# Optimization experiments

Hardware: AMD Instinct MI355X
Metric: run time of the kernel (lower is better)

## Reference

```python
import jax, jax.numpy as jnp
import numpy as np

B, H, W, C, NBHD, T, OUT_DIM = 4, 96, 96, 256, 48, 3025, 512
N = H * W
INNER = 4
DS_RATE = 0.25


def _layer_norm(x, w, b, eps=1e-5):
    mu = jnp.mean(x, axis=-1, keepdims=True)
    var = jnp.mean((x - mu) ** 2, axis=-1, keepdims=True)
    return (x - mu) * jax.lax.rsqrt(var + eps) * w + b


def setup_inputs() -> dict:
    key = jax.random.key(0)
    ks = jax.random.split(key, 8)
    # regular grid positions: pos % 4 == 0 (both dims) on exactly 24*24=576 tokens
    yy, xx = jnp.meshgrid(jnp.arange(H), jnp.arange(W), indexing='ij')
    pos = jnp.stack([yy, xx], axis=-1).reshape(1, N, 2).astype(jnp.float32)
    pos = jnp.broadcast_to(pos, (B, N, 2))
    feat = jax.random.normal(ks[0], (B, N, C), dtype=jnp.float32)
    member_idx = jax.random.randint(ks[1], (B, N, NBHD), 0, N)
    cluster_mask = (jax.random.uniform(ks[2], (B, N, NBHD)) > 0.1).astype(jnp.float32)
    learned_prob = jax.random.uniform(ks[3], (B, N, 1), dtype=jnp.float32)
    pe_idx = jax.random.randint(ks[4], (B, N, NBHD), 0, T)
    pre_table = jax.random.normal(ks[5], (T, 5), dtype=jnp.float32)
    # weight_net: Linear(5,4) + LayerNorm(4) + GELU
    w1 = jax.random.normal(ks[6], (5, INNER), dtype=jnp.float32) * 0.3
    b1 = jnp.zeros((INNER,), jnp.float32)
    ln1_w = jnp.ones((INNER,), jnp.float32)
    ln1_b = jnp.zeros((INNER,), jnp.float32)
    # norm over inner_ch*dim, then Linear(inner_ch*dim -> out_dim)
    norm_w = jnp.ones((INNER * C,), jnp.float32)
    norm_b = jnp.zeros((INNER * C,), jnp.float32)
    lin_w = jax.random.normal(ks[7], (INNER * C, OUT_DIM), dtype=jnp.float32) * 0.02
    lin_b = jnp.zeros((OUT_DIM,), jnp.float32)
    return {
        'pos': pos, 'feat': feat, 'member_idx': member_idx,
        'cluster_mask': cluster_mask, 'learned_prob': learned_prob,
        'pe_idx': pe_idx, 'pre_table': pre_table,
        'w1': w1, 'b1': b1, 'ln1_w': ln1_w, 'ln1_b': ln1_b,
        'norm_w': norm_w, 'norm_b': norm_b, 'lin_w': lin_w, 'lin_b': lin_b,
        'stride': 2, 'reserve_num': 576,
    }


def reference(pos, feat, member_idx, cluster_mask, learned_prob, pe_idx,
              pre_table, w1, b1, ln1_w, ln1_b, norm_w, norm_b, lin_w, lin_b,
              stride, reserve_num):
    b, n, c = feat.shape
    nbhd = member_idx.shape[-1]
    keep_num = int(n * DS_RATE)
    sample_num = keep_num - reserve_num

    pos_long = pos.astype(jnp.int32)
    lp_det = jax.lax.stop_gradient(learned_prob[..., 0])  # b x n (detached in torch)
    reserve_mask = jnp.all(pos_long % (stride * 2) == 0, axis=-1).astype(jnp.float32)
    final_prob = lp_det + reserve_mask * (-100.0)

    # topk sampled tokens (reserved tokens pushed to -100 so never sampled)
    sample_idx = jax.lax.top_k(final_prob, sample_num)[1]  # b x sample_num
    # reserved token indices in ascending index order (torch nonzero order)
    reserve_idx = jnp.argsort(-reserve_mask, axis=1, stable=True)[:, :reserve_num]
    idx = jnp.concatenate([sample_idx, reserve_idx], axis=1)  # b x keep_num

    pos_down = jnp.take_along_axis(pos, idx[:, :, None], axis=1)  # b x keep x 2

    member_d = jnp.take_along_axis(member_idx, idx[:, :, None], axis=1)   # b x keep x nbhd
    pe_d = jnp.take_along_axis(pe_idx, idx[:, :, None], axis=1)
    cmask_d = jnp.take_along_axis(cluster_mask, idx[:, :, None], axis=1)

    flat_mi = member_d.reshape(b, keep_num * nbhd)
    # gather learned prob of each neighbor (NOT detached: grads flow)
    lp_nb = jnp.take_along_axis(learned_prob, flat_mi[:, :, None], axis=1)
    lp_nb = lp_nb.reshape(b, keep_num, nbhd, 1)

    # weight_net over pre-computed position table -> T x inner_ch
    wt = jax.nn.gelu(_layer_norm(pre_table @ w1 + b1, ln1_w, ln1_b))
    weights = wt[pe_d]  # b x keep x nbhd x inner_ch
    weights = weights * (lp_nb * cmask_d[..., None])

    # gather neighbor features and do position-weighted aggregation
    feat_g = jnp.take_along_axis(feat, flat_mi[:, :, None], axis=1)
    feat_g = feat_g.reshape(b, keep_num, nbhd, c)
    feat_down = jnp.einsum('bnkm,bnkc->bnmc', weights, feat_g)
    feat_down = feat_down.reshape(b, keep_num, INNER * c)

    feat_down = _layer_norm(feat_down, norm_w, norm_b)
    feat_down = feat_down @ lin_w + lin_b
    return pos_down, feat_down
```

## Files before the change

kernel.cpp:

```cpp
#include <hip/hip_runtime.h>
#include <hip/hip_bf16.h>
#include <stdint.h>

#define BB 4
#define NN 9216
#define CC 256
#define NBHD 48
#define T_TAB 3025
#define OUT_DIM 512
#define KEEP 2304
#define RESERVE 576
#define SAMPLE 1728
#define W_IMG 96

typedef __attribute__((ext_vector_type(4))) float f32x4;
typedef __attribute__((ext_vector_type(8))) short s16x8;

__device__ inline unsigned short f2bf_bits(float x) {
    __hip_bfloat16 h = __float2bfloat16(x);
    return __builtin_bit_cast(unsigned short, h);
}

__global__ void wt_kernel(const float* __restrict__ pre_table,
                          const float* __restrict__ w1,
                          const float* __restrict__ b1,
                          const float* __restrict__ ln1w,
                          const float* __restrict__ ln1b,
                          float* __restrict__ wt) {
    int t = blockIdx.x * blockDim.x + threadIdx.x;
    if (t >= T_TAB) return;
    float p[5];
#pragma unroll
    for (int j = 0; j < 5; j++) p[j] = pre_table[t * 5 + j];
    float h[4];
#pragma unroll
    for (int m = 0; m < 4; m++) {
        float a = b1[m];
#pragma unroll
        for (int j = 0; j < 5; j++) a += p[j] * w1[j * 4 + m];
        h[m] = a;
    }
    float mu = 0.25f * (h[0] + h[1] + h[2] + h[3]);
    float var = 0.f;
#pragma unroll
    for (int m = 0; m < 4; m++) { float d = h[m] - mu; var += d * d; }
    var *= 0.25f;
    float rs = rsqrtf(var + 1e-5f);
#pragma unroll
    for (int m = 0; m < 4; m++) {
        float x = (h[m] - mu) * rs * ln1w[m] + ln1b[m];
        float u = 0.7978845608028654f * (x + 0.044715f * x * x * x);
        wt[t * 4 + m] = 0.5f * x * (1.0f + tanhf(u));
    }
}

#define JSPLIT 8
#define JCHUNK (NN / JSPLIT)
__device__ inline float final_prob(const float* f, int i) {
    int y = i / W_IMG, x = i % W_IMG;
    bool res = ((y & 3) == 0) && ((x & 3) == 0);
    return f[i] + (res ? -100.0f : 0.0f);
}
__global__ __launch_bounds__(256) void rank_kernel(const float* __restrict__ lp,
                                                   int* __restrict__ rank) {
    __shared__ float s[JCHUNK];
    int b = blockIdx.z;
    int i = blockIdx.x * 256 + threadIdx.x;
    int jbase = blockIdx.y * JCHUNK;
    const float* f = lp + b * NN;
    for (int j = threadIdx.x; j < JCHUNK; j += 256)
        s[j] = final_prob(f, jbase + j);
    __syncthreads();
    float fi = final_prob(f, i);
    int cnt = 0;
#pragma unroll 8
    for (int jj = 0; jj < JCHUNK; jj++) {
        float fj = s[jj];
        int j = jbase + jj;
        cnt += (int)((fj > fi) || (fj == fi && j < i));
    }
    atomicAdd(&rank[b * NN + i], cnt);
}

__global__ void scatter_kernel(const float* __restrict__ pos,
                               const int* __restrict__ rank,
                               int* __restrict__ idx,
                               float* __restrict__ pos_down) {
    int g = blockIdx.x * 256 + threadIdx.x;
    if (g >= BB * NN) return;
    int b = g / NN, i = g % NN;
    float py = pos[g * 2 + 0], px = pos[g * 2 + 1];
    int y = (int)py, x = (int)px;
    bool res = ((y & 3) == 0) && ((x & 3) == 0);
    int slot = -1;
    if (res) {
        slot = SAMPLE + (y >> 2) * (W_IMG / 4) + (x >> 2);
    } else {
        int r = rank[g];
        if (r < SAMPLE) slot = r;
    }
    if (slot >= 0) {
        idx[b * KEEP + slot] = i;
        pos_down[(b * KEEP + slot) * 2 + 0] = py;
        pos_down[(b * KEEP + slot) * 2 + 1] = px;
    }
}

__global__ void feat2bf_kernel(const float* __restrict__ f,
                               unsigned short* __restrict__ o) {
    int g = blockIdx.x * 256 + threadIdx.x;
    float4 v = ((const float4*)f)[g];
    ushort4 u;
    u.x = f2bf_bits(v.x); u.y = f2bf_bits(v.y);
    u.z = f2bf_bits(v.z); u.w = f2bf_bits(v.w);
    ((ushort4*)o)[g] = u;
}

__global__ __launch_bounds__(256) void wtrans_kernel(const float* __restrict__ W,
                                                     __hip_bfloat16* __restrict__ Wt) {
    __shared__ float s[32][33];
    int bx = blockIdx.x;
    int by = blockIdx.y;
    int tx = threadIdx.x & 31, ty = threadIdx.x >> 5;
#pragma unroll
    for (int r = 0; r < 4; r++)
        s[ty * 4 + r][tx] = W[(size_t)(by * 32 + ty * 4 + r) * 512 + bx * 32 + tx];
    __syncthreads();
#pragma unroll
    for (int r = 0; r < 4; r++)
        Wt[(size_t)(bx * 32 + ty * 4 + r) * 1024 + by * 32 + tx] =
            __float2bfloat16(s[tx][ty * 4 + r]);
}

__device__ inline float ldf(const float* p) { return *p; }
__device__ inline float ldf(const __hip_bfloat16* p) { return __bfloat162float(*p); }

template <typename FT>
__global__ __launch_bounds__(256) void agg_kernel(
        const FT* __restrict__ feat,
        const int* __restrict__ member_idx,
        const float* __restrict__ cmask,
        const float* __restrict__ lp,
        const int* __restrict__ pe_idx,
        const float* __restrict__ wt,
        const int* __restrict__ idx,
        const float* __restrict__ norm_w,
        const float* __restrict__ norm_b,
        __hip_bfloat16* __restrict__ xnorm) {
    int t = blockIdx.x, b = blockIdx.y, tid = threadIdx.x;
    __shared__ int s_mem[NBHD];
    __shared__ float s_w[NBHD * 4];
    __shared__ float s_red[8];
    int i = idx[b * KEEP + t];
    if (tid < NBHD) {
        size_t base = ((size_t)b * NN + i) * NBHD + tid;
        int mi = member_idx[base];
        int pe = pe_idx[base];
        float fsc = lp[b * NN + mi] * cmask[base];
        s_mem[tid] = mi;
        s_w[tid * 4 + 0] = wt[pe * 4 + 0] * fsc;
        s_w[tid * 4 + 1] = wt[pe * 4 + 1] * fsc;
        s_w[tid * 4 + 2] = wt[pe * 4 + 2] * fsc;
        s_w[tid * 4 + 3] = wt[pe * 4 + 3] * fsc;
    }
    __syncthreads();
    float a0 = 0.f, a1 = 0.f, a2 = 0.f, a3 = 0.f;
    const FT* fb = feat + (size_t)b * NN * CC + tid;
#pragma unroll 4
    for (int k = 0; k < NBHD; k++) {
        float fv = ldf(fb + (size_t)s_mem[k] * CC);
        a0 += s_w[k * 4 + 0] * fv;
        a1 += s_w[k * 4 + 1] * fv;
        a2 += s_w[k * 4 + 2] * fv;
        a3 += s_w[k * 4 + 3] * fv;
    }
    float s1 = a0 + a1 + a2 + a3;
    float s2 = a0 * a0 + a1 * a1 + a2 * a2 + a3 * a3;
    for (int off = 32; off > 0; off >>= 1) {
        s1 += __shfl_down(s1, off);
        s2 += __shfl_down(s2, off);
    }
    int wid = tid >> 6;
    if ((tid & 63) == 0) { s_red[wid] = s1; s_red[4 + wid] = s2; }
    __syncthreads();
    float S1 = s_red[0] + s_red[1] + s_red[2] + s_red[3];
    float S2 = s_red[4] + s_red[5] + s_red[6] + s_red[7];
    float mu = S1 * (1.0f / 1024.0f);
    float var = S2 * (1.0f / 1024.0f) - mu * mu;
    float rs = rsqrtf(var + 1e-5f);
    __hip_bfloat16* xo = xnorm + ((size_t)(b * KEEP + t)) * 1024;
#pragma unroll
    for (int m = 0; m < 4; m++) {
        float am = (m == 0) ? a0 : (m == 1) ? a1 : (m == 2) ? a2 : a3;
        int c = m * 256 + tid;
        xo[c] = __float2bfloat16((am - mu) * rs * norm_w[c] + norm_b[c]);
    }
}

__device__ inline void async16(const void* g, void* l) {
    __builtin_amdgcn_global_load_lds(
        (const __attribute__((address_space(1))) void*)g,
        (__attribute__((address_space(3))) void*)l, 16, 0, 0);
}
__device__ inline void mfma16x16x32(f32x4& d, const s16x8& a, const s16x8& b) {
    asm("v_mfma_f32_16x16x32_bf16 %0, %1, %2, %0" : "+v"(d) : "v"(a), "v"(b));
}

__global__ __launch_bounds__(256) void mfma_gemm(
        const __hip_bfloat16* __restrict__ A,
        const __hip_bfloat16* __restrict__ Bt,
        const float* __restrict__ bias,
        float* __restrict__ Cout) {
    __shared__ __hip_bfloat16 sA[128 * 32];
    __shared__ __hip_bfloat16 sB[128 * 32];
    int tid = threadIdx.x;
    int wave = tid >> 6, lane = tid & 63;
    int wm = wave >> 1, wn = wave & 1;
    int row0 = blockIdx.y * 128, col0 = blockIdx.x * 128;

    int lrow = lane >> 2;
    int lcol = (lane & 3) * 8;
    const __hip_bfloat16* gA = A + (size_t)(row0 + wave * 32 + lrow) * 1024 + lcol;
    const __hip_bfloat16* gB = Bt + (size_t)(col0 + wave * 32 + lrow) * 1024 + lcol;
    __hip_bfloat16* lA0 = sA + (wave * 32) * 32;
    __hip_bfloat16* lA1 = sA + (wave * 32 + 16) * 32;
    __hip_bfloat16* lB0 = sB + (wave * 32) * 32;
    __hip_bfloat16* lB1 = sB + (wave * 32 + 16) * 32;

    f32x4 acc[4][4] = {};
    int fr = lane & 15;
    int fq = lane >> 4;

    for (int kk = 0; kk < 1024; kk += 32) {
        async16(gA + kk, lA0);
        async16(gA + kk + 16 * 1024, lA1);
        async16(gB + kk, lB0);
        async16(gB + kk + 16 * 1024, lB1);
        __syncthreads();
        s16x8 af[4], bf[4];
#pragma unroll
        for (int i = 0; i < 4; i++)
            af[i] = *(const s16x8*)(sA + (wm * 64 + i * 16 + fr) * 32 + fq * 8);
#pragma unroll
        for (int j = 0; j < 4; j++)
            bf[j] = *(const s16x8*)(sB + (wn * 64 + j * 16 + fr) * 32 + fq * 8);
#pragma unroll
        for (int i = 0; i < 4; i++)
#pragma unroll
            for (int j = 0; j < 4; j++)
                mfma16x16x32(acc[i][j], af[i], bf[j]);
        __syncthreads();
    }
    asm volatile("s_nop 7\ns_nop 7" ::);
    float bv[4];
#pragma unroll
    for (int j = 0; j < 4; j++) bv[j] = bias[col0 + wn * 64 + j * 16 + fr];
#pragma unroll
    for (int i = 0; i < 4; i++) {
        int row = row0 + wm * 64 + i * 16 + fq * 4;
#pragma unroll
        for (int j = 0; j < 4; j++) {
            int col = col0 + wn * 64 + j * 16 + fr;
            float* cp = Cout + (size_t)row * 512 + col;
#pragma unroll
            for (int r = 0; r < 4; r++)
                cp[(size_t)r * 512] = acc[i][j][r] + bv[j];
        }
    }
}

extern "C" void kernel_launch(void* const* d_in, const int* in_sizes, int n_in,
                              void* d_out, int out_size, void* d_ws, size_t ws_size,
                              hipStream_t stream) {
    const float* pos       = (const float*)d_in[0];
    const float* feat      = (const float*)d_in[1];
    const int*   member_idx= (const int*)d_in[2];
    const float* cmask     = (const float*)d_in[3];
    const float* lp        = (const float*)d_in[4];
    const int*   pe_idx    = (const int*)d_in[5];
    const float* pre_table = (const float*)d_in[6];
    const float* w1        = (const float*)d_in[7];
    const float* b1        = (const float*)d_in[8];
    const float* ln1w      = (const float*)d_in[9];
    const float* ln1b      = (const float*)d_in[10];
    const float* norm_w    = (const float*)d_in[11];
    const float* norm_b    = (const float*)d_in[12];
    const float* lin_w     = (const float*)d_in[13];
    const float* lin_b     = (const float*)d_in[14];

    float* out = (float*)d_out;
    float* pos_down = out;
    float* feat_out = out + (size_t)BB * KEEP * 2;

    char* ws = (char*)d_ws;
    float*          wt     = (float*)(ws + 0);
    int*            rank   = (int*)  (ws + 48640);
    int*            idx    = (int*)  (ws + 196096);
    __hip_bfloat16* wtb    = (__hip_bfloat16*)(ws + 232960);
    __hip_bfloat16* xnormb = (__hip_bfloat16*)(ws + 1281536);
    __hip_bfloat16* featb  = (__hip_bfloat16*)(ws + 20155904);
    const size_t NEED_BF16FEAT = 20155904 + 18874368;
    bool use_bf16_feat = (ws_size >= NEED_BF16FEAT);

    wt_kernel<<<dim3((T_TAB + 255) / 256), 256, 0, stream>>>(pre_table, w1, b1, ln1w, ln1b, wt);
    hipMemsetAsync(rank, 0, (size_t)BB * NN * 4, stream);
    rank_kernel<<<dim3(NN / 256, JSPLIT, BB), 256, 0, stream>>>(lp, rank);
    scatter_kernel<<<dim3((BB * NN) / 256), 256, 0, stream>>>(pos, rank, idx, pos_down);
    wtrans_kernel<<<dim3(512 / 32, 1024 / 32), 256, 0, stream>>>(lin_w, wtb);
    if (use_bf16_feat) {
        feat2bf_kernel<<<dim3((BB * NN * CC / 4) / 256), 256, 0, stream>>>(feat, (unsigned short*)featb);
        agg_kernel<__hip_bfloat16><<<dim3(KEEP, BB), 256, 0, stream>>>(
            featb, member_idx, cmask, lp, pe_idx, wt, idx, norm_w, norm_b, xnormb);
    } else {
        agg_kernel<float><<<dim3(KEEP, BB), 256, 0, stream>>>(
            feat, member_idx, cmask, lp, pe_idx, wt, idx, norm_w, norm_b, xnormb);
    }
    mfma_gemm<<<dim3(OUT_DIM / 128, (BB * KEEP) / 128), 256, 0, stream>>>(xnormb, wtb, lin_b, feat_out);
}
```

Before: 254.1 us.

## Replace all-pairs rank with histogram threshold and candidate ranking for top-k

Replaces the O(N^2) all-pairs rank counting over every token with a radix-histogram top-k selection. A 16-bit key histogram sets a threshold bin, candidates at or above it are gathered with atomics, and only those candidates are ranked pairwise. Positions are now derived from the token index instead of read from pos. This relies on the candidate count staying under CAND_CAP, which learned_prob values clustered in one bin could exceed, and it adds several small serial launches.

Result: slower. 355.8 us (+40.0%).

```diff
diff --git a/kernel.cpp b/kernel.cpp
--- a/kernel.cpp
+++ b/kernel.cpp
@@ -12,6 +12,7 @@
 #define RESERVE 576
 #define SAMPLE 1728
 #define W_IMG 96
+#define CAND_CAP 6144
 
 typedef __attribute__((ext_vector_type(4))) float f32x4;
 typedef __attribute__((ext_vector_type(8))) short s16x8;
@@ -19,6 +20,16 @@
 __device__ inline unsigned short f2bf_bits(float x) {
     __hip_bfloat16 h = __float2bfloat16(x);
     return __builtin_bit_cast(unsigned short, h);
+}
+
+__device__ inline unsigned int fkey(float v) {
+    unsigned int u = __builtin_bit_cast(unsigned int, v);
+    return (u & 0x80000000u) ? ~u : (u | 0x80000000u);
+}
+__device__ inline float final_prob_val(const float* lpb, int i) {
+    int y = i / W_IMG, x = i % W_IMG;
+    bool res = ((y & 3) == 0) && ((x & 3) == 0);
+    return lpb[i] + (res ? -100.0f : 0.0f);
 }
 
 __global__ void wt_kernel(const float* __restrict__ pre_table,
@@ -54,55 +65,108 @@
     }
 }
 
-#define JSPLIT 8
-#define JCHUNK (NN / JSPLIT)
-__device__ inline float final_prob(const float* f, int i) {
-    int y = i / W_IMG, x = i % W_IMG;
-    bool res = ((y & 3) == 0) && ((x & 3) == 0);
-    return f[i] + (res ? -100.0f : 0.0f);
-}
-__global__ __launch_bounds__(256) void rank_kernel(const float* __restrict__ lp,
-                                                   int* __restrict__ rank) {
-    __shared__ float s[JCHUNK];
-    int b = blockIdx.z;
-    int i = blockIdx.x * 256 + threadIdx.x;
-    int jbase = blockIdx.y * JCHUNK;
-    const float* f = lp + b * NN;
-    for (int j = threadIdx.x; j < JCHUNK; j += 256)
-        s[j] = final_prob(f, jbase + j);
+__global__ void hist_kernel(const float* __restrict__ lp,
+                            int* __restrict__ hist) {
+    int g = blockIdx.x * 256 + threadIdx.x;
+    if (g >= BB * NN) return;
+    int b = g / NN, i = g % NN;
+    float v = final_prob_val(lp + b * NN, i);
+    unsigned int bin = fkey(v) >> 16;
+    atomicAdd(&hist[b * 65536 + bin], 1);
+}
+
+__global__ __launch_bounds__(256) void thresh_kernel(const int* __restrict__ hist,
+                                                     int* __restrict__ thr) {
+    int b = blockIdx.x, t = threadIdx.x;
+    __shared__ int part[256];
+    const int* h = hist + b * 65536;
+    int lo = 65536 - (t + 1) * 256;
+    int sum = 0;
+    for (int k = 0; k < 256; k++) sum += h[lo + k];
+    part[t] = sum;
     __syncthreads();
-    float fi = final_prob(f, i);
-    int cnt = 0;
-#pragma unroll 8
-    for (int jj = 0; jj < JCHUNK; jj++) {
-        float fj = s[jj];
-        int j = jbase + jj;
-        cnt += (int)((fj > fi) || (fj == fi && j < i));
-    }
-    atomicAdd(&rank[b * NN + i], cnt);
-}
-
-__global__ void scatter_kernel(const float* __restrict__ pos,
-                               const int* __restrict__ rank,
+    if (t == 0) {
+        int cum = 0, T = 0;
+        for (int r = 0; r < 256; r++) {
+            if (cum + part[r] >= SAMPLE) {
+                int lo2 = 65536 - (r + 1) * 256;
+                int c = cum;
+                for (int bin = 65536 - r * 256 - 1; bin >= lo2; bin--) {
+                    c += h[bin];
+                    if (c >= SAMPLE) { T = bin; break; }
+                }
+                break;
+            }
+            cum += part[r];
+        }
+        thr[b] = T;
+    }
+}
+
+__global__ void collect_kernel(const float* __restrict__ lp,
+                               const int* __restrict__ thr,
+                               int* __restrict__ cnt,
+                               float* __restrict__ cand_val,
+                               int* __restrict__ cand_idx,
                                int* __restrict__ idx,
                                float* __restrict__ pos_down) {
     int g = blockIdx.x * 256 + threadIdx.x;
     if (g >= BB * NN) return;
     int b = g / NN, i = g % NN;
-    float py = pos[g * 2 + 0], px = pos[g * 2 + 1];
-    int y = (int)py, x = (int)px;
+    int y = i / W_IMG, x = i % W_IMG;
     bool res = ((y & 3) == 0) && ((x & 3) == 0);
-    int slot = -1;
     if (res) {
-        slot = SAMPLE + (y >> 2) * (W_IMG / 4) + (x >> 2);
+        int slot = SAMPLE + (y >> 2) * (W_IMG / 4) + (x >> 2);
+        idx[b * KEEP + slot] = i;
+        pos_down[(b * KEEP + slot) * 2 + 0] = (float)y;
+        pos_down[(b * KEEP + slot) * 2 + 1] = (float)x;
     } else {
-        int r = rank[g];
-        if (r < SAMPLE) slot = r;
-    }
-    if (slot >= 0) {
-        idx[b * KEEP + slot] = i;
-        pos_down[(b * KEEP + slot) * 2 + 0] = py;
-        pos_down[(b * KEEP + slot) * 2 + 1] = px;
+        float v = lp[g];
+        if ((int)(fkey(v) >> 16) >= thr[b]) {
+            int p = atomicAdd(&cnt[b], 1);
+            if (p < CAND_CAP) {
+                cand_val[b * CAND_CAP + p] = v;
+                cand_idx[b * CAND_CAP + p] = i;
+            }
+        }
+    }
+}
+
+#define RCHUNK 2048
+__global__ __launch_bounds__(256) void rank_cand_kernel(
+        const int* __restrict__ cnt,
+        const float* __restrict__ cand_val,
+        const int* __restrict__ cand_idx,
+        int* __restrict__ idx,
+        float* __restrict__ pos_down) {
+    __shared__ float sv[RCHUNK];
+    __shared__ int si[RCHUNK];
+    int b = blockIdx.y;
+    int C = cnt[b]; if (C > CAND_CAP) C = CAND_CAP;
+    int i = blockIdx.x * 256 + threadIdx.x;
+    bool valid = (i < C);
+    float vi = 0.f; int ii = 0;
+    if (valid) { vi = cand_val[b * CAND_CAP + i]; ii = cand_idx[b * CAND_CAP + i]; }
+    int rank = 0;
+    for (int base = 0; base < C; base += RCHUNK) {
+        int len = min(RCHUNK, C - base);
+        for (int j = threadIdx.x; j < len; j += 256) {
+            sv[j] = cand_val[b * CAND_CAP + base + j];
+            si[j] = cand_idx[b * CAND_CAP + base + j];
+        }
+        __syncthreads();
+        if (valid) {
+            for (int j = 0; j < len; j++) {
+                float vj = sv[j];
+                rank += (int)((vj > vi) || (vj == vi && si[j] < ii));
+            }
+        }
+        __syncthreads();
+    }
+    if (valid && rank < SAMPLE) {
+        idx[b * KEEP + rank] = ii;
+        pos_down[(b * KEEP + rank) * 2 + 0] = (float)(ii / W_IMG);
+        pos_down[(b * KEEP + rank) * 2 + 1] = (float)(ii % W_IMG);
     }
 }
 
@@ -294,18 +358,24 @@
 
     char* ws = (char*)d_ws;
     float*          wt     = (float*)(ws + 0);
-    int*            rank   = (int*)  (ws + 48640);
-    int*            idx    = (int*)  (ws + 196096);
-    __hip_bfloat16* wtb    = (__hip_bfloat16*)(ws + 232960);
-    __hip_bfloat16* xnormb = (__hip_bfloat16*)(ws + 1281536);
-    __hip_bfloat16* featb  = (__hip_bfloat16*)(ws + 20155904);
-    const size_t NEED_BF16FEAT = 20155904 + 18874368;
+    int*            hist   = (int*)  (ws + 48640);
+    int*            ccnt   = (int*)  (ws + 1097216);
+    int*            thr    = (int*)  (ws + 1097472);
+    float*          cval   = (float*)(ws + 1097728);
+    int*            cidx   = (int*)  (ws + 1196032);
+    int*            idx    = (int*)  (ws + 1294336);
+    __hip_bfloat16* wtb    = (__hip_bfloat16*)(ws + 1331200);
+    __hip_bfloat16* xnormb = (__hip_bfloat16*)(ws + 2379776);
+    __hip_bfloat16* featb  = (__hip_bfloat16*)(ws + 21254144);
+    const size_t NEED_BF16FEAT = 21254144 + 18874368;
     bool use_bf16_feat = (ws_size >= NEED_BF16FEAT);
 
     wt_kernel<<<dim3((T_TAB + 255) / 256), 256, 0, stream>>>(pre_table, w1, b1, ln1w, ln1b, wt);
-    hipMemsetAsync(rank, 0, (size_t)BB * NN * 4, stream);
-    rank_kernel<<<dim3(NN / 256, JSPLIT, BB), 256, 0, stream>>>(lp, rank);
-    scatter_kernel<<<dim3((BB * NN) / 256), 256, 0, stream>>>(pos, rank, idx, pos_down);
+    hipMemsetAsync(hist, 0, 1048576 + 256, stream);
+    hist_kernel<<<dim3((BB * NN) / 256), 256, 0, stream>>>(lp, hist);
+    thresh_kernel<<<dim3(BB), 256, 0, stream>>>(hist, thr);
+    collect_kernel<<<dim3((BB * NN) / 256), 256, 0, stream>>>(lp, thr, ccnt, cval, cidx, idx, pos_down);
+    rank_cand_kernel<<<dim3(CAND_CAP / 256, BB), 256, 0, stream>>>(ccnt, cval, cidx, idx, pos_down);
     wtrans_kernel<<<dim3(512 / 32, 1024 / 32), 256, 0, stream>>>(lin_w, wtb);
     if (use_bf16_feat) {
         feat2bf_kernel<<<dim3((BB * NN * CC / 4) / 256), 256, 0, stream>>>(feat, (unsigned short*)featb);
```
